# Kernel optimization log

Hardware: AMD Instinct MI355X
Metric: run time of the kernel (lower is better)

## Reference

```python
import jax, jax.numpy as jnp
import numpy as np

C = 256  # channels
SHAPES = [(8, C, 80, 80), (8, C, 40, 40), (8, C, 20, 20), (8, C, 10, 10)]
EPS = 1e-8  # torch cosine_similarity eps


def _nearest_resize(x, H, W):
    # Matches F.interpolate(mode='nearest'): src_idx = floor(dst_idx * in/out)
    b, c, h, w = x.shape
    rows = (jnp.arange(H) * h) // H
    cols = (jnp.arange(W) * w) // W
    return x[:, :, rows[:, None], cols[None, :]]


def setup_inputs() -> dict:
    key = jax.random.key(0)
    ks = jax.random.split(key, 12)
    d = {}
    for i, s in enumerate(SHAPES):
        d[f"f{i}"] = jax.random.normal(ks[i], s, dtype=jnp.float32)
        d[f"w{i}"] = jax.random.normal(ks[4 + i], (C, C), dtype=jnp.float32) / jnp.sqrt(jnp.float32(C))
        d[f"b{i}"] = jax.random.normal(ks[8 + i], (C,), dtype=jnp.float32) * 0.01
    return d


def reference(f0, f1, f2, f3, w0, w1, w2, w3, b0, b1, b2, b3):
    feats = [f0, f1, f2, f3]
    ws = [w0, w1, w2, w3]
    bs = [b0, b1, b2, b3]
    H = max(f.shape[2] for f in feats)
    W = max(f.shape[3] for f in feats)
    proj = []
    for f, w, b in zip(feats, ws, bs):
        # 1x1 conv == per-pixel GEMM over channels
        p = jnp.einsum('bchw,oc->bohw', f, w) + b[None, :, None, None]
        if p.shape[2] != H or p.shape[3] != W:
            p = _nearest_resize(p, H, W)
        proj.append(p)
    B = proj[0].shape[0]
    N = len(proj)
    x = jnp.stack(proj, axis=1).reshape(B, N, C, H * W)  # [B,N,C,L]
    # Pairwise cosine similarity along channel dim at each spatial location,
    # then mean over locations (vectorized form of the O(N^2) torch loop).
    dot = jnp.einsum('bicl,bjcl->bijl', x, x)            # [B,N,N,L]
    nrm = jnp.sqrt(jnp.einsum('bicl,bicl->bil', x, x))   # [B,N,L]
    denom = jnp.maximum(nrm[:, :, None, :] * nrm[:, None, :, :], EPS)
    attn = (dot / denom).mean(axis=-1)                   # [B,N,N]
    return jax.nn.softmax(attn, axis=-1)
```

## Files before the change

### kernel.cpp

```cpp
#include <hip/hip_runtime.h>


#define CCH 256
#define WPITCH 40

typedef __attribute__((ext_vector_type(8))) short short8;
typedef __attribute__((ext_vector_type(4))) short short4_;
typedef __attribute__((ext_vector_type(4))) float float4_;

__device__ inline short f2bf(float x) {
    union { float f; unsigned u; } c; c.f = x;
    unsigned u = c.u + 0x7FFFu + ((c.u >> 16) & 1u);
    return (short)(u >> 16);
}
__device__ inline float bf2f(short b) {
    union { unsigned u; float f; } c; c.u = ((unsigned)(unsigned short)b) << 16;
    return c.f;
}

__device__ inline void dma16(const void* g, void* l) {
    __builtin_amdgcn_global_load_lds(
        (const __attribute__((address_space(1))) void*)g,
        (__attribute__((address_space(3))) void*)l, 16, 0, 0);
}

__global__ __launch_bounds__(256) void proj_small(
    const float* __restrict__ f1, const float* __restrict__ f2,
    const float* __restrict__ f3,
    const float* __restrict__ w0, const float* __restrict__ w1,
    const float* __restrict__ w2, const float* __restrict__ w3,
    const float* __restrict__ b1, const float* __restrict__ b2,
    const float* __restrict__ b3,
    short* __restrict__ u1, short* __restrict__ u2, short* __restrict__ u3,
    short* __restrict__ wp)
{
    __shared__ __align__(16) short Wt[256 * WPITCH];
    __shared__ __align__(16) short Ft[64 * WPITCH];

    const int blk = blockIdx.x;
    const int t = threadIdx.x;

    if (blk >= 272) {
        int id = (blk - 272) * 256 + t;
        int ks = id >> 10;
        int rest = id & 1023;
        int mt = rest >> 6;
        int fl = rest & 63;
        int ln = fl & 15, qd = fl >> 4;
        const float* src = w0 + (size_t)(mt * 16 + ln) * CCH + ks * 32 + qd * 8;
        short8 v;
#pragma unroll
        for (int j = 0; j < 8; ++j) v[j] = f2bf(src[j]);
        *(short8*)(wp + (size_t)id * 8) = v;
        return;
    }

    int b, tile, L;
    const float* F; const float* Wg; const float* bias; short* U;
    if (blk < 200)      { int r = blk;       b = r / 25; tile = r % 25; L = 1600; F = f1; Wg = w1; bias = b1; U = u1; }
    else if (blk < 256) { int r = blk - 200; b = r / 7;  tile = r % 7;  L = 400;  F = f2; Wg = w2; bias = b2; U = u2; }
    else                { int r = blk - 256; b = r / 2;  tile = r % 2;  L = 100;  F = f3; Wg = w3; bias = b3; U = u3; }

    const int lane = t & 63;
    const int wav  = t >> 6;
    const int ln   = lane & 15;
    const int quad = lane >> 4;
    const int pixbase = tile * 64;
    const float* Fb = F + (size_t)b * CCH * L;

    const int wo = t >> 2;
    const int wk = (t & 3) * 8;
    const int fpix = t & 63;
    const int fchunk = t >> 6;
    const int gpix0 = pixbase + fpix;
    const bool pin = gpix0 < L;
    const int gl0 = pin ? gpix0 : 0;

    float4_ wbufA[4], wbufB[4];
    float fbuf[8];
    auto loadW = [&](int ks) {
#pragma unroll
        for (int p = 0; p < 4; ++p) {
            const float* srcp = Wg + (size_t)(p * 64 + wo) * CCH + ks * 32 + wk;
            wbufA[p] = *(const float4_*)srcp;
            wbufB[p] = *(const float4_*)(srcp + 4);
        }
    };
    auto loadF = [&](int ks) {
        const float* fs = Fb + (size_t)(ks * 32 + fchunk * 8) * L + gl0;
#pragma unroll
        for (int j = 0; j < 8; ++j) fbuf[j] = fs[(size_t)j * L];
    };

    float4_ acc[16];
#pragma unroll
    for (int i = 0; i < 16; ++i) acc[i] = (float4_){0.f, 0.f, 0.f, 0.f};

    loadW(0); loadF(0);
    for (int ks = 0; ks < 8; ++ks) {
        __syncthreads();
#pragma unroll
        for (int p = 0; p < 4; ++p) {
            short8 v;
#pragma unroll
            for (int e = 0; e < 4; ++e) { v[e] = f2bf(wbufA[p][e]); v[e + 4] = f2bf(wbufB[p][e]); }
            *(short8*)(&Wt[(p * 64 + wo) * WPITCH + wk]) = v;
        }
        {
            short8 v;
#pragma unroll
            for (int j = 0; j < 8; ++j) v[j] = pin ? f2bf(fbuf[j]) : (short)0;
            *(short8*)(&Ft[fpix * WPITCH + fchunk * 8]) = v;
        }
        __syncthreads();
        const int ksn = (ks + 1) & 7;
        loadW(ksn); loadF(ksn);

        short8 bfrag = *(const short8*)(&Ft[(wav * 16 + ln) * WPITCH + quad * 8]);
#pragma unroll
        for (int mt = 0; mt < 16; ++mt) {
            short8 afrag = *(const short8*)(&Wt[(mt * 16 + ln) * WPITCH + quad * 8]);
            acc[mt] = __builtin_amdgcn_mfma_f32_16x16x32_bf16(afrag, bfrag, acc[mt], 0, 0, 0);
        }
    }

    float ss = 0.f;
#pragma unroll
    for (int mt = 0; mt < 16; ++mt) {
        float4_ bv = *(const float4_*)(bias + mt * 16 + quad * 4);
#pragma unroll
        for (int r = 0; r < 4; ++r) { float v = acc[mt][r] + bv[r]; acc[mt][r] = v; ss += v * v; }
    }
    ss += __shfl_xor(ss, 16);
    ss += __shfl_xor(ss, 32);
    const float inv = 1.f / sqrtf(fmaxf(ss, 1e-24f));

    const int gpixw = pixbase + wav * 16 + ln;
    if (gpixw < L) {
        short* dst = U + ((size_t)b * L + gpixw) * CCH;
#pragma unroll
        for (int mt = 0; mt < 16; ++mt) {
            short4_ v;
#pragma unroll
            for (int r = 0; r < 4; ++r) v[r] = f2bf(acc[mt][r] * inv);
            *(short4_*)(dst + mt * 16 + quad * 4) = v;
        }
    }
}

__global__ __launch_bounds__(512) void proj0_dots(
    const float* __restrict__ F, const short* __restrict__ wp,
    const float* __restrict__ bias,
    const short* __restrict__ u1, const short* __restrict__ u2,
    const short* __restrict__ u3,
    float* __restrict__ partial)
{
    __shared__ __align__(16) char smem[65536];
    short* Wb0 = (short*)smem;
    short* Wb1 = (short*)(smem + 16384);
    float* Fb0 = (float*)(smem + 32768);
    float* Fb1 = (float*)(smem + 49152);
    short* S1 = (short*)smem;
    short* S2 = (short*)(smem + 16384);
    short* S3 = (short*)(smem + 20480);
    float* redF = (float*)(smem + 24576);
    float* redC = (float*)(smem + 24576 + 96);

    const int c  = blockIdx.x;
    const int b  = blockIdx.y;
    const int R  = c / 5, C = c - R * 5;
    const int t  = threadIdx.x;
    const int lane = t & 63;
    const int wav  = t >> 6;
    const int ln   = lane & 15;
    const int quad = lane >> 4;
    const float* Fbase = F + (size_t)b * CCH * 6400;

    auto dmaW = [&](int ks, int buf) {
        short* Wb = buf ? Wb1 : Wb0;
#pragma unroll
        for (int m = 0; m < 2; ++m) {
            const int k = wav * 2 + m;
            const short* g = wp + (size_t)ks * 8192 + k * 512 + lane * 8;
            dma16(g, Wb + k * 512);
        }
    };
    auto dmaF = [&](int ks, int buf) {
        float* Fb = buf ? Fb1 : Fb0;
#pragma unroll
        for (int m = 0; m < 2; ++m) {
            const int k = wav * 2 + m;
            const int chl = 2 * k + (lane >> 5);
            const int px4 = (lane & 31) * 4;
            const int gpx = (8 * R + (px4 >> 4)) * 80 + 16 * C + (px4 & 15);
            const float* g = Fbase + (size_t)(ks * 32 + chl) * 6400 + gpx;
            dma16(g, Fb + k * 256);
        }
    };

    float4_ acc[16];
#pragma unroll
    for (int i = 0; i < 16; ++i) acc[i] = (float4_){0.f, 0.f, 0.f, 0.f};

    const int pxme = wav * 16 + ln;

    dmaW(0, 0); dmaF(0, 0);
    for (int ks = 0; ks < 8; ++ks) {
        __syncthreads();
        if (ks < 7) { dmaW(ks + 1, (ks + 1) & 1); dmaF(ks + 1, (ks + 1) & 1); }
        const short* Wl = (ks & 1) ? Wb1 : Wb0;
        const float* Fl = (ks & 1) ? Fb1 : Fb0;
        short8 bfrag;
#pragma unroll
        for (int j = 0; j < 8; ++j)
            bfrag[j] = f2bf(Fl[(quad * 8 + j) * 128 + pxme]);
#pragma unroll
        for (int mt = 0; mt < 16; ++mt) {
            short8 afrag = *(const short8*)(Wl + mt * 512 + lane * 8);
            acc[mt] = __builtin_amdgcn_mfma_f32_16x16x32_bf16(afrag, bfrag, acc[mt], 0, 0, 0);
        }
    }

    float ss = 0.f;
#pragma unroll
    for (int mt = 0; mt < 16; ++mt) {
        float4_ bv = *(const float4_*)(bias + mt * 16 + quad * 4);
#pragma unroll
        for (int r = 0; r < 4; ++r) { float v = acc[mt][r] + bv[r]; acc[mt][r] = v; ss += v * v; }
    }
    ss += __shfl_xor(ss, 16);
    ss += __shfl_xor(ss, 32);
    const float inv = 1.f / sqrtf(fmaxf(ss, 1e-24f));

    __syncthreads();

    {
        const int p1 = t >> 4, ck = (t & 15) * 16;
        const int lr = p1 >> 3, lc = p1 & 7;
        const short* src = u1 + ((size_t)(b * 1600 + (4 * R + lr) * 40 + 8 * C + lc)) * CCH + ck;
        *(short8*)(&S1[p1 * 256 + ck])     = *(const short8*)src;
        *(short8*)(&S1[p1 * 256 + ck + 8]) = *(const short8*)(src + 8);
    }
    if (t < 128) {
        const int p2 = t >> 4, ck = (t & 15) * 16;
        const int lr = p2 >> 2, lc = p2 & 3;
        const short* src = u2 + ((size_t)(b * 400 + (2 * R + lr) * 20 + 4 * C + lc)) * CCH + ck;
        *(short8*)(&S2[p2 * 256 + ck])     = *(const short8*)src;
        *(short8*)(&S2[p2 * 256 + ck + 8]) = *(const short8*)(src + 8);
    }
    if (t < 32) {
        const int p3 = t >> 4, ck = (t & 15) * 16;
        const short* src = u3 + ((size_t)(b * 100 + R * 10 + 2 * C + p3)) * CCH + ck;
        *(short8*)(&S3[p3 * 256 + ck])     = *(const short8*)src;
        *(short8*)(&S3[p3 * 256 + ck + 8]) = *(const short8*)(src + 8);
    }
    __syncthreads();

    const int pr = pxme >> 4, pc = pxme & 15;
    const int c1l = (pr >> 1) * 8 + (pc >> 1);
    const int c2l = (pr >> 2) * 4 + (pc >> 2);
    const int c3l = pc >> 3;
    float d01 = 0.f, d02 = 0.f, d03 = 0.f;
#pragma unroll
    for (int mt = 0; mt < 16; ++mt) {
        const int ch = mt * 16 + quad * 4;
        short4_ v1 = *(const short4_*)(&S1[c1l * 256 + ch]);
        short4_ v2 = *(const short4_*)(&S2[c2l * 256 + ch]);
        short4_ v3 = *(const short4_*)(&S3[c3l * 256 + ch]);
#pragma unroll
        for (int r = 0; r < 4; ++r) {
            float a = acc[mt][r] * inv;
            d01 += a * bf2f(v1[r]);
            d02 += a * bf2f(v2[r]);
            d03 += a * bf2f(v3[r]);
        }
    }
    {
        float vals[3] = {d01, d02, d03};
#pragma unroll
        for (int p = 0; p < 3; ++p) {
            float v = vals[p];
            v += __shfl_xor(v, 1);  v += __shfl_xor(v, 2);  v += __shfl_xor(v, 4);
            v += __shfl_xor(v, 8);  v += __shfl_xor(v, 16); v += __shfl_xor(v, 32);
            if (lane == 0) redF[wav * 3 + p] = v;
        }
    }

    if (wav < 2) {
        const int p1 = wav * 16 + (lane >> 2);
        const int q  = lane & 3;
        const int lr = p1 >> 3, lc = p1 & 7;
        const int par2 = (lr >> 1) * 4 + (lc >> 1);
        const int par3 = lc >> 2;
        float e12 = 0.f, e13 = 0.f;
#pragma unroll
        for (int k = 0; k < 16; ++k) {
            short4_ a1 = *(const short4_*)(&S1[p1 * 256 + q * 64 + k * 4]);
            short4_ a2 = *(const short4_*)(&S2[par2 * 256 + q * 64 + k * 4]);
            short4_ a3 = *(const short4_*)(&S3[par3 * 256 + q * 64 + k * 4]);
#pragma unroll
            for (int r = 0; r < 4; ++r) {
                float x1 = bf2f(a1[r]);
                e12 += x1 * bf2f(a2[r]);
                e13 += x1 * bf2f(a3[r]);
            }
        }
        float ev[2] = {e12, e13};
#pragma unroll
        for (int p = 0; p < 2; ++p) {
            float v = ev[p];
            v += __shfl_xor(v, 1);  v += __shfl_xor(v, 2);  v += __shfl_xor(v, 4);
            v += __shfl_xor(v, 8);  v += __shfl_xor(v, 16); v += __shfl_xor(v, 32);
            if (lane == 0) redC[wav * 2 + p] = v;
        }
    } else if (wav == 2) {
        float e23 = 0.f;
        if (lane < 32) {
            const int p2 = lane >> 2;
            const int q  = lane & 3;
            const int par3 = (p2 & 3) >> 1;
#pragma unroll
            for (int k = 0; k < 16; ++k) {
                short4_ a2 = *(const short4_*)(&S2[p2 * 256 + q * 64 + k * 4]);
                short4_ a3 = *(const short4_*)(&S3[par3 * 256 + q * 64 + k * 4]);
#pragma unroll
                for (int r = 0; r < 4; ++r) e23 += bf2f(a2[r]) * bf2f(a3[r]);
            }
        }
        e23 += __shfl_xor(e23, 1);  e23 += __shfl_xor(e23, 2);  e23 += __shfl_xor(e23, 4);
        e23 += __shfl_xor(e23, 8);  e23 += __shfl_xor(e23, 16); e23 += __shfl_xor(e23, 32);
        if (lane == 0) redC[4] = e23;
    }
    __syncthreads();

    if (t < 6) {
        float v;
        if (t < 3) {
            v = 0.f;
#pragma unroll
            for (int w = 0; w < 8; ++w) v += redF[w * 3 + t];
        } else if (t == 3) v = redC[0] + redC[2];
        else if (t == 4)   v = redC[1] + redC[3];
        else               v = redC[4];
        partial[((size_t)b * 6 + t) * 50 + c] = v;
    }
}

__global__ void softmax4(const float* __restrict__ partial, float* __restrict__ out) {
    int t = threadIdx.x;
    if (t >= 128) return;
    int b = t >> 4, i = (t >> 2) & 3, j = t & 3;
    float a[4];
#pragma unroll
    for (int jj = 0; jj < 4; ++jj) {
        if (jj == i) { a[jj] = 1.0f; continue; }
        int lo = i < jj ? i : jj;
        int hi = i < jj ? jj : i;
        int pidx;
        if (lo == 0) pidx = hi - 1;
        else if (lo == 1) pidx = 1 + hi;
        else pidx = 5;
        const float* pp = partial + ((size_t)b * 6 + pidx) * 50;
        float s = 0.f;
        for (int k = 0; k < 50; ++k) s += pp[k];
        int rf = 80 >> lo;
        a[jj] = s / (float)(rf * rf);
    }
    float m = fmaxf(fmaxf(a[0], a[1]), fmaxf(a[2], a[3]));
    float e0 = expf(a[0] - m), e1 = expf(a[1] - m), e2 = expf(a[2] - m), e3 = expf(a[3] - m);
    float sum = e0 + e1 + e2 + e3;
    float ev = (j == 0) ? e0 : (j == 1) ? e1 : (j == 2) ? e2 : e3;
    out[t] = ev / sum;
}

extern "C" void kernel_launch(void* const* d_in, const int* in_sizes, int n_in,
                              void* d_out, int out_size, void* d_ws, size_t ws_size,
                              hipStream_t stream) {
    const float* f[4]  = {(const float*)d_in[0], (const float*)d_in[3],
                          (const float*)d_in[6], (const float*)d_in[9]};
    const float* w[4]  = {(const float*)d_in[1], (const float*)d_in[4],
                          (const float*)d_in[7], (const float*)d_in[10]};
    const float* bs[4] = {(const float*)d_in[2], (const float*)d_in[5],
                          (const float*)d_in[8], (const float*)d_in[11]};

    char* ws = (char*)d_ws;
    size_t off = 0;
    short* u1 = (short*)(ws + off); off += (size_t)8 * CCH * 1600 * sizeof(short);
    short* u2 = (short*)(ws + off); off += (size_t)8 * CCH * 400  * sizeof(short);
    short* u3 = (short*)(ws + off); off += (size_t)8 * CCH * 100  * sizeof(short);
    short* wp = (short*)(ws + off); off += (size_t)65536 * sizeof(short);
    float* partial = (float*)(ws + off);

    proj_small<<<304, 256, 0, stream>>>(f[1], f[2], f[3],
                                        w[0], w[1], w[2], w[3],
                                        bs[1], bs[2], bs[3],
                                        u1, u2, u3, wp);

    proj0_dots<<<dim3(50, 8), 512, 0, stream>>>(f[0], wp, bs[0],
                                                u1, u2, u3, partial);

    softmax4<<<1, 128, 0, stream>>>(partial, (float*)d_out);
}
```

Before: 159.3 us.

## Halve proj0 tile to 4x16 pixels, drop double buffering, double grid

Each proj0_dots block now covers a 4x16 pixel tile with 256 threads instead of an 8x16 tile with 512 threads, so the grid grows to 100x8 blocks. The double-buffered W/F staging is replaced by a single buffer with a sync before and after each DMA stage, which cuts LDS use from 64 KB to about 24 KB. The aim is more resident blocks per CU and better spread across CUs, so other blocks can hide the load latency. In exchange, W is reloaded twice as often in total and the load/compute overlap inside each block is lost. The partial buffer is widened to 100 entries, and softmax4 is updated to sum over them.

```diff
diff --git a/kernel.cpp b/kernel.cpp
--- a/kernel.cpp
+++ b/kernel.cpp
@@ -148,27 +148,25 @@
     }
 }
 
-__global__ __launch_bounds__(512) void proj0_dots(
+__global__ __launch_bounds__(256) void proj0_dots(
     const float* __restrict__ F, const short* __restrict__ wp,
     const float* __restrict__ bias,
     const short* __restrict__ u1, const short* __restrict__ u2,
     const short* __restrict__ u3,
     float* __restrict__ partial)
 {
-    __shared__ __align__(16) char smem[65536];
-    short* Wb0 = (short*)smem;
-    short* Wb1 = (short*)(smem + 16384);
-    float* Fb0 = (float*)(smem + 32768);
-    float* Fb1 = (float*)(smem + 49152);
+    __shared__ __align__(16) char smem[24576 + 256];
+    short* Wb = (short*)smem;
+    float* Fb = (float*)(smem + 16384);
     short* S1 = (short*)smem;
-    short* S2 = (short*)(smem + 16384);
-    short* S3 = (short*)(smem + 20480);
-    float* redF = (float*)(smem + 24576);
-    float* redC = (float*)(smem + 24576 + 96);
+    short* S2 = (short*)(smem + 8192);
+    short* S3 = (short*)(smem + 10240);
+    float* redF = (float*)(smem + 11264);
+    float* redC = (float*)(smem + 11264 + 48);
 
     const int c  = blockIdx.x;
     const int b  = blockIdx.y;
-    const int R  = c / 5, C = c - R * 5;
+    const int RB = c / 5, CB = c - RB * 5;
     const int t  = threadIdx.x;
     const int lane = t & 63;
     const int wav  = t >> 6;
@@ -176,27 +174,23 @@
     const int quad = lane >> 4;
     const float* Fbase = F + (size_t)b * CCH * 6400;
 
-    auto dmaW = [&](int ks, int buf) {
-        short* Wb = buf ? Wb1 : Wb0;
+    auto dmaW = [&](int ks) {
+#pragma unroll
+        for (int m = 0; m < 4; ++m) {
+            const int k = wav * 4 + m;
+            dma16(wp + (size_t)ks * 8192 + k * 512 + lane * 8, Wb + k * 512);
+        }
+    };
+    auto dmaF = [&](int ks) {
 #pragma unroll
         for (int m = 0; m < 2; ++m) {
             const int k = wav * 2 + m;
-            const short* g = wp + (size_t)ks * 8192 + k * 512 + lane * 8;
-            dma16(g, Wb + k * 512);
+            const int ch = k * 4 + (lane >> 4);
+            const int px4 = (lane & 15) * 4;
+            const int gpx = (4 * RB + (px4 >> 4)) * 80 + 16 * CB + (px4 & 15);
+            dma16(Fbase + (size_t)(ks * 32 + ch) * 6400 + gpx, Fb + k * 256);
         }
     };
-    auto dmaF = [&](int ks, int buf) {
-        float* Fb = buf ? Fb1 : Fb0;
-#pragma unroll
-        for (int m = 0; m < 2; ++m) {
-            const int k = wav * 2 + m;
-            const int chl = 2 * k + (lane >> 5);
-            const int px4 = (lane & 31) * 4;
-            const int gpx = (8 * R + (px4 >> 4)) * 80 + 16 * C + (px4 & 15);
-            const float* g = Fbase + (size_t)(ks * 32 + chl) * 6400 + gpx;
-            dma16(g, Fb + k * 256);
-        }
-    };
 
     float4_ acc[16];
 #pragma unroll
@@ -204,19 +198,17 @@
 
     const int pxme = wav * 16 + ln;
 
-    dmaW(0, 0); dmaF(0, 0);
     for (int ks = 0; ks < 8; ++ks) {
         __syncthreads();
-        if (ks < 7) { dmaW(ks + 1, (ks + 1) & 1); dmaF(ks + 1, (ks + 1) & 1); }
-        const short* Wl = (ks & 1) ? Wb1 : Wb0;
-        const float* Fl = (ks & 1) ? Fb1 : Fb0;
+        dmaW(ks); dmaF(ks);
+        __syncthreads();
         short8 bfrag;
 #pragma unroll
         for (int j = 0; j < 8; ++j)
-            bfrag[j] = f2bf(Fl[(quad * 8 + j) * 128 + pxme]);
+            bfrag[j] = f2bf(Fb[(quad * 8 + j) * 64 + pxme]);
 #pragma unroll
         for (int mt = 0; mt < 16; ++mt) {
-            short8 afrag = *(const short8*)(Wl + mt * 512 + lane * 8);
+            short8 afrag = *(const short8*)(Wb + mt * 512 + lane * 8);
             acc[mt] = __builtin_amdgcn_mfma_f32_16x16x32_bf16(afrag, bfrag, acc[mt], 0, 0, 0);
         }
     }
@@ -237,20 +229,19 @@
     {
         const int p1 = t >> 4, ck = (t & 15) * 16;
         const int lr = p1 >> 3, lc = p1 & 7;
-        const short* src = u1 + ((size_t)(b * 1600 + (4 * R + lr) * 40 + 8 * C + lc)) * CCH + ck;
+        const short* src = u1 + ((size_t)(b * 1600 + (2 * RB + lr) * 40 + 8 * CB + lc)) * CCH + ck;
         *(short8*)(&S1[p1 * 256 + ck])     = *(const short8*)src;
         *(short8*)(&S1[p1 * 256 + ck + 8]) = *(const short8*)(src + 8);
     }
-    if (t < 128) {
+    if (t < 64) {
         const int p2 = t >> 4, ck = (t & 15) * 16;
-        const int lr = p2 >> 2, lc = p2 & 3;
-        const short* src = u2 + ((size_t)(b * 400 + (2 * R + lr) * 20 + 4 * C + lc)) * CCH + ck;
+        const short* src = u2 + ((size_t)(b * 400 + RB * 20 + 4 * CB + p2)) * CCH + ck;
         *(short8*)(&S2[p2 * 256 + ck])     = *(const short8*)src;
         *(short8*)(&S2[p2 * 256 + ck + 8]) = *(const short8*)(src + 8);
     }
     if (t < 32) {
         const int p3 = t >> 4, ck = (t & 15) * 16;
-        const short* src = u3 + ((size_t)(b * 100 + R * 10 + 2 * C + p3)) * CCH + ck;
+        const short* src = u3 + ((size_t)(b * 100 + (RB >> 1) * 10 + 2 * CB + p3)) * CCH + ck;
         *(short8*)(&S3[p3 * 256 + ck])     = *(const short8*)src;
         *(short8*)(&S3[p3 * 256 + ck + 8]) = *(const short8*)(src + 8);
     }
@@ -258,7 +249,7 @@
 
     const int pr = pxme >> 4, pc = pxme & 15;
     const int c1l = (pr >> 1) * 8 + (pc >> 1);
-    const int c2l = (pr >> 2) * 4 + (pc >> 2);
+    const int c2l = pc >> 2;
     const int c3l = pc >> 3;
     float d01 = 0.f, d02 = 0.f, d03 = 0.f;
 #pragma unroll
@@ -286,11 +277,10 @@
         }
     }
 
-    if (wav < 2) {
-        const int p1 = wav * 16 + (lane >> 2);
-        const int q  = lane & 3;
-        const int lr = p1 >> 3, lc = p1 & 7;
-        const int par2 = (lr >> 1) * 4 + (lc >> 1);
+    if (wav == 0) {
+        const int p1 = lane >> 2, q = lane & 3;
+        const int lc = p1 & 7;
+        const int par2 = lc >> 1;
         const int par3 = lc >> 2;
         float e12 = 0.f, e13 = 0.f;
 #pragma unroll
@@ -311,14 +301,13 @@
             float v = ev[p];
             v += __shfl_xor(v, 1);  v += __shfl_xor(v, 2);  v += __shfl_xor(v, 4);
             v += __shfl_xor(v, 8);  v += __shfl_xor(v, 16); v += __shfl_xor(v, 32);
-            if (lane == 0) redC[wav * 2 + p] = v;
-        }
-    } else if (wav == 2) {
+            if (lane == 0) redC[p] = v;
+        }
+    } else if (wav == 1) {
         float e23 = 0.f;
-        if (lane < 32) {
-            const int p2 = lane >> 2;
-            const int q  = lane & 3;
-            const int par3 = (p2 & 3) >> 1;
+        if (lane < 16) {
+            const int p2 = lane >> 2, q = lane & 3;
+            const int par3 = p2 >> 1;
 #pragma unroll
             for (int k = 0; k < 16; ++k) {
                 short4_ a2 = *(const short4_*)(&S2[p2 * 256 + q * 64 + k * 4]);
@@ -329,20 +318,16 @@
         }
         e23 += __shfl_xor(e23, 1);  e23 += __shfl_xor(e23, 2);  e23 += __shfl_xor(e23, 4);
         e23 += __shfl_xor(e23, 8);  e23 += __shfl_xor(e23, 16); e23 += __shfl_xor(e23, 32);
-        if (lane == 0) redC[4] = e23;
+        if (lane == 0) redC[2] = e23;
     }
     __syncthreads();
 
     if (t < 6) {
         float v;
         if (t < 3) {
-            v = 0.f;
-#pragma unroll
-            for (int w = 0; w < 8; ++w) v += redF[w * 3 + t];
-        } else if (t == 3) v = redC[0] + redC[2];
-        else if (t == 4)   v = redC[1] + redC[3];
-        else               v = redC[4];
-        partial[((size_t)b * 6 + t) * 50 + c] = v;
+            v = redF[t] + redF[3 + t] + redF[6 + t] + redF[9 + t];
+        } else v = redC[t - 3];
+        partial[((size_t)b * 6 + t) * 100 + c] = v;
     }
 }
 
@@ -360,9 +345,9 @@
         if (lo == 0) pidx = hi - 1;
         else if (lo == 1) pidx = 1 + hi;
         else pidx = 5;
-        const float* pp = partial + ((size_t)b * 6 + pidx) * 50;
+        const float* pp = partial + ((size_t)b * 6 + pidx) * 100;
         float s = 0.f;
-        for (int k = 0; k < 50; ++k) s += pp[k];
+        for (int k = 0; k < 100; ++k) s += pp[k];
         int rf = 80 >> lo;
         a[jj] = s / (float)(rf * rf);
     }
@@ -396,8 +381,8 @@
                                         bs[1], bs[2], bs[3],
                                         u1, u2, u3, wp);
 
-    proj0_dots<<<dim3(50, 8), 512, 0, stream>>>(f[0], wp, bs[0],
-                                                u1, u2, u3, partial);
+    proj0_dots<<<dim3(100, 8), 256, 0, stream>>>(f[0], wp, bs[0],
+                                                 u1, u2, u3, partial);
 
     softmax4<<<1, 128, 0, stream>>>(partial, (float*)d_out);
 }
```

Result: no change. 161.7 us (+1.5%).
